# Optimization experiments

Hardware: AMD Instinct MI355X
Metric: run time of the kernel (lower is better)

## Reference

```python
import jax, jax.numpy as jnp
import numpy as np

D_MODEL = 512
NH_ATTN = 8
D_STATE = 64
HEADDIM = 128
D_INNER = 2 * D_MODEL          # 1024
NHEADS = D_INNER // HEADDIM    # 8
CONV_K = 4
CONV_DIM = D_INNER + 2 * D_STATE            # 1152
D_IN_PROJ = 2 * D_INNER + 2 * D_STATE + NHEADS  # 2184
B, S, M = 2, 2048, 1024
EPS = 1e-5


def setup_inputs() -> dict:
    key = jax.random.key(0)
    ks = jax.random.split(key, 10)
    s = 0.02
    return {
        'x': jax.random.normal(ks[0], (B, S, D_MODEL), dtype=jnp.float32),
        'memory': jax.random.normal(ks[1], (B, M, D_MODEL), dtype=jnp.float32),
        'pad_mask': jnp.ones((B, S, 1), dtype=jnp.float32),
        'ln1_g': jnp.ones((D_MODEL,)), 'ln1_b': jnp.zeros((D_MODEL,)),
        'ln2_g': jnp.ones((D_MODEL,)), 'ln2_b': jnp.zeros((D_MODEL,)),
        'W_in': jax.random.normal(ks[2], (D_IN_PROJ, D_MODEL)) * s,
        'conv_w': jax.random.normal(ks[3], (CONV_DIM, 1, CONV_K)) * s,
        'conv_b': jnp.zeros((CONV_DIM,)),
        'dt_bias': jnp.log(jnp.expm1(jax.random.uniform(ks[4], (NHEADS,), minval=0.001, maxval=0.1))),
        'A_log': jnp.log(jnp.arange(1, NHEADS + 1, dtype=jnp.float32)),
        'D_skip': jnp.ones((NHEADS,)),
        'rms_w': jnp.ones((D_INNER,)),
        'W_out': jax.random.normal(ks[5], (D_MODEL, D_INNER)) * s,
        'Wqkv': jax.random.normal(ks[6], (3 * D_MODEL, D_MODEL)) * s,
        'bqkv': jnp.zeros((3 * D_MODEL,)),
        'Wo': jax.random.normal(ks[7], (D_MODEL, D_MODEL)) * s,
        'bo': jnp.zeros((D_MODEL,)),
    }


def _layernorm(x, g, b):
    m = jnp.mean(x, axis=-1, keepdims=True)
    v = jnp.mean((x - m) ** 2, axis=-1, keepdims=True)
    return (x - m) * jax.lax.rsqrt(v + EPS) * g + b


def _mamba(x, W_in, conv_w, conv_b, dt_bias, A_log, D_skip, rms_w, W_out):
    b, s, _ = x.shape
    zxbcdt = x @ W_in.T                                     # [b,s,2184]
    z, xBC, dt = jnp.split(zxbcdt, [D_INNER, D_INNER + CONV_DIM], axis=-1)
    # causal depthwise conv over time on (x, B, C)
    xt = jnp.transpose(xBC, (0, 2, 1))                      # [b,C,s]
    xt = jax.lax.conv_general_dilated(
        xt, conv_w, (1,), [(CONV_K - 1, 0)],
        feature_group_count=CONV_DIM,
        dimension_numbers=('NCH', 'OIH', 'NCH'))
    xBC = jax.nn.silu(jnp.transpose(xt, (0, 2, 1)) + conv_b)
    xs, Bm, Cm = jnp.split(xBC, [D_INNER, D_INNER + D_STATE], axis=-1)
    dt = jax.nn.softplus(dt + dt_bias)                      # [b,s,H]
    A = -jnp.exp(A_log)                                     # [H]
    xh = xs.reshape(b, s, NHEADS, HEADDIM)                  # [b,s,H,P]

    def step(h, inps):
        dt_t, B_t, C_t, x_t = inps                          # [b,H],[b,N],[b,N],[b,H,P]
        decay = jnp.exp(dt_t * A)                           # [b,H]
        h = h * decay[..., None, None] + (dt_t[..., None, None] * x_t[..., None]) * B_t[:, None, None, :]
        y = jnp.einsum('bhpn,bn->bhp', h, C_t)
        return h, y

    h0 = jnp.zeros((b, NHEADS, HEADDIM, D_STATE), dtype=x.dtype)
    _, ys = jax.lax.scan(step, h0, (dt.transpose(1, 0, 2), Bm.transpose(1, 0, 2),
                                    Cm.transpose(1, 0, 2), xh.transpose(1, 0, 2, 3)))
    y = ys.transpose(1, 0, 2, 3) + D_skip[None, None, :, None] * xh
    y = y.reshape(b, s, D_INNER) * jax.nn.silu(z)           # gated
    y = y * jax.lax.rsqrt(jnp.mean(y * y, axis=-1, keepdims=True) + EPS) * rms_w
    return y @ W_out.T


def _cross_attn(q_in, memory, Wqkv, bqkv, Wo, bo):
    b, s, _ = q_in.shape
    m = memory.shape[1]
    dh = D_MODEL // NH_ATTN
    q = (q_in @ Wqkv[:D_MODEL].T + bqkv[:D_MODEL]).reshape(b, s, NH_ATTN, dh)
    k = (memory @ Wqkv[D_MODEL:2 * D_MODEL].T + bqkv[D_MODEL:2 * D_MODEL]).reshape(b, m, NH_ATTN, dh)
    v = (memory @ Wqkv[2 * D_MODEL:].T + bqkv[2 * D_MODEL:]).reshape(b, m, NH_ATTN, dh)
    scores = jnp.einsum('bqhd,bkhd->bhqk', q, k) / jnp.sqrt(jnp.asarray(dh, q.dtype))
    p = jax.nn.softmax(scores, axis=-1)
    out = jnp.einsum('bhqk,bkhd->bqhd', p, v).reshape(b, s, D_MODEL)
    return out @ Wo.T + bo


def reference(x, memory, pad_mask, ln1_g, ln1_b, ln2_g, ln2_b, W_in, conv_w, conv_b,
              dt_bias, A_log, D_skip, rms_w, W_out, Wqkv, bqkv, Wo, bo):
    residual = x
    xn = _layernorm(x, ln1_g, ln1_b) * pad_mask
    x = residual + _mamba(xn, W_in, conv_w, conv_b, dt_bias, A_log, D_skip, rms_w, W_out)
    h = _layernorm(x, ln2_g, ln2_b)
    x = x + _cross_attn(h, memory, Wqkv, bqkv, Wo, bo)
    return x
```

## Files before the change

kernel.cpp:

```cpp
#include <hip/hip_runtime.h>
#include <hip/hip_bf16.h>

typedef __hip_bfloat16 bf16;
typedef short v8s __attribute__((ext_vector_type(8)));
typedef short v4s __attribute__((ext_vector_type(4)));
typedef float v4f __attribute__((ext_vector_type(4)));

__device__ __forceinline__ void gll16(const bf16* g, bf16* l) {
    __builtin_amdgcn_global_load_lds(
        (const __attribute__((address_space(1))) unsigned int*)g,
        (__attribute__((address_space(3))) unsigned int*)l, 16, 0, 0);
}
__device__ __forceinline__ float bf2f(short s) {
    return __uint_as_float(((unsigned int)(unsigned short)s) << 16);
}
__device__ __forceinline__ short f2bfs(float f) {
    return (short)__bfloat16_as_ushort(__float2bfloat16(f));
}

__global__ __launch_bounds__(256) void pre_kernel(
    const float* __restrict__ x, const float* __restrict__ g,
    const float* __restrict__ bt, const float* __restrict__ mask,
    bf16* __restrict__ xn,
    const float* __restrict__ W_in, const float* __restrict__ W_out,
    const float* __restrict__ Wqkv, const float* __restrict__ Wo,
    const float* __restrict__ mem,
    bf16* __restrict__ Winb, bf16* __restrict__ Woutb, bf16* __restrict__ Wqkvb,
    bf16* __restrict__ Wob, bf16* __restrict__ memb)
{
    int tid = threadIdx.x;
    if (blockIdx.x < 4096) {
        int row = blockIdx.x;
        const float* xr = x + (size_t)row * 512;
        float v0 = xr[tid], v1 = xr[tid + 256];
        float s = v0 + v1, ss = v0 * v0 + v1 * v1;
        #pragma unroll
        for (int o = 32; o; o >>= 1) { s += __shfl_xor(s, o); ss += __shfl_xor(ss, o); }
        __shared__ float l1[4], l2[4];
        if ((tid & 63) == 0) { l1[tid >> 6] = s; l2[tid >> 6] = ss; }
        __syncthreads();
        s = l1[0] + l1[1] + l1[2] + l1[3];
        ss = l2[0] + l2[1] + l2[2] + l2[3];
        float mean = s * (1.f / 512.f);
        float var = ss * (1.f / 512.f) - mean * mean;
        float rs = rsqrtf(var + 1e-5f);
        float mk = mask[row];
        xn[(size_t)row * 512 + tid] =
            __float2bfloat16(((v0 - mean) * rs * g[tid] + bt[tid]) * mk);
        xn[(size_t)row * 512 + tid + 256] =
            __float2bfloat16(((v1 - mean) * rs * g[tid + 256] + bt[tid + 256]) * mk);
        return;
    }
    int i = (blockIdx.x - 4096) * 256 + tid;
    const int E0 = 2184 * 512;
    const int E1 = E0 + 524288;
    const int E2 = E1 + 786432;
    const int E3 = E2 + 262144;
    const int E4 = E3 + 1048576;
    if (i < E0) {
        Winb[i] = __float2bfloat16(W_in[i]);
    } else if (i < E1) {
        int j = i - E0; Woutb[j] = __float2bfloat16(W_out[j]);
    } else if (i < E2) {
        int j = i - E1; Wqkvb[j] = __float2bfloat16(Wqkv[j]);
    } else if (i < E3) {
        int j = i - E2; Wob[j] = __float2bfloat16(Wo[j]);
    } else if (i < E4) {
        int j = i - E3; memb[j] = __float2bfloat16(mem[j]);
    }
}

__global__ __launch_bounds__(256) void ln_kernel(
    const bf16* __restrict__ x, const float* __restrict__ g,
    const float* __restrict__ bt, bf16* __restrict__ out)
{
    int row = blockIdx.x, tid = threadIdx.x;
    const bf16* xr = x + (size_t)row * 512;
    unsigned int pk = *(const unsigned int*)(xr + tid * 2);
    float v0 = bf2f((short)(pk & 0xffff));
    float v1 = bf2f((short)(pk >> 16));
    float s = v0 + v1, ss = v0 * v0 + v1 * v1;
    #pragma unroll
    for (int o = 32; o; o >>= 1) { s += __shfl_xor(s, o); ss += __shfl_xor(ss, o); }
    __shared__ float l1[4], l2[4];
    if ((tid & 63) == 0) { l1[tid >> 6] = s; l2[tid >> 6] = ss; }
    __syncthreads();
    s = l1[0] + l1[1] + l1[2] + l1[3];
    ss = l2[0] + l2[1] + l2[2] + l2[3];
    float mean = s * (1.f / 512.f);
    float var = ss * (1.f / 512.f) - mean * mean;
    float rs = rsqrtf(var + 1e-5f);
    int i0 = tid * 2;
    unsigned int po =
        (unsigned int)(unsigned short)f2bfs((v0 - mean) * rs * g[i0] + bt[i0]) |
        ((unsigned int)(unsigned short)f2bfs((v1 - mean) * rs * g[i0 + 1] + bt[i0 + 1]) << 16);
    *(unsigned int*)(out + (size_t)row * 512 + i0) = po;
}

__global__ __launch_bounds__(256) void gemm_in(
    const bf16* __restrict__ A, const bf16* __restrict__ W, bf16* __restrict__ C)
{
    __shared__ bf16 lA[2][64 * 32];
    __shared__ bf16 lB[2][128 * 32];
    int bm = blockIdx.x * 64, bn = blockIdx.y * 128;
    int tid = threadIdx.x, lane = tid & 63, wv = tid >> 6;
    int wc = wv * 32;
    int lr15 = lane & 15, l4 = lane >> 4, lk8 = (lane >> 4) * 8;

    v4f acc[4][2] = {};
    int sr = tid >> 2, sc = (tid & 3) * 8;
    const bf16* Abase = A + (size_t)(bm + sr) * 512 + sc;
    const bf16* Wbase = W + (size_t)(bn + sr) * 512 + sc;

    int cur = 0;
    gll16(Abase, &lA[0][tid * 8]);
    gll16(Wbase, &lB[0][tid * 8]);
    gll16(Wbase + (size_t)64 * 512, &lB[0][tid * 8 + 2048]);
    __syncthreads();
    for (int t = 0; t < 16; ++t) {
        if (t + 1 < 16) {
            int k0 = (t + 1) * 32;
            gll16(Abase + k0, &lA[cur ^ 1][tid * 8]);
            gll16(Wbase + k0, &lB[cur ^ 1][tid * 8]);
            gll16(Wbase + (size_t)64 * 512 + k0, &lB[cur ^ 1][tid * 8 + 2048]);
        }
        v8s af[4], bfr[2];
        #pragma unroll
        for (int mi = 0; mi < 4; ++mi)
            af[mi] = *(const v8s*)&lA[cur][(mi * 16 + lr15) * 32 + lk8];
        #pragma unroll
        for (int ni = 0; ni < 2; ++ni)
            bfr[ni] = *(const v8s*)&lB[cur][(wc + ni * 16 + lr15) * 32 + lk8];
        #pragma unroll
        for (int mi = 0; mi < 4; ++mi)
            #pragma unroll
            for (int ni = 0; ni < 2; ++ni)
                acc[mi][ni] = __builtin_amdgcn_mfma_f32_16x16x32_bf16(
                    af[mi], bfr[ni], acc[mi][ni], 0, 0, 0);
        __syncthreads();
        cur ^= 1;
    }
    #pragma unroll
    for (int mi = 0; mi < 4; ++mi) {
        #pragma unroll
        for (int ni = 0; ni < 2; ++ni) {
            int col = bn + wc + ni * 16 + lr15;
            if (col < 2184) {
                #pragma unroll
                for (int r = 0; r < 4; ++r) {
                    int row = bm + mi * 16 + l4 * 4 + r;
                    C[(size_t)row * 2184 + col] = __float2bfloat16(acc[mi][ni][r]);
                }
            }
        }
    }
}

__global__ __launch_bounds__(256) void gemm64(
    const bf16* __restrict__ Aall, const bf16* __restrict__ Wall,
    const float* __restrict__ bias, const void* __restrict__ resid,
    void* __restrict__ Cout,
    int M, int N, int K, int ldA, int ldW, int ldC,
    long sA1, long sA2, long sW1, long sW2, long sC1, long sC2,
    int zdiv, int outbf16, int residbf16, bf16* __restrict__ vTout)
{
    __shared__ bf16 lA[2][64 * 32];
    __shared__ bf16 lB[2][64 * 32];
    int z = blockIdx.z;
    int zb = z / zdiv, zh = z - zb * zdiv;
    const bf16* A = Aall + zb * sA1 + zh * sA2;
    const bf16* W = Wall + zb * sW1 + zh * sW2;
    long coff = zb * sC1 + zh * sC2;

    int bm = blockIdx.x * 64, bn = blockIdx.y * 64;
    int tid = threadIdx.x, lane = tid & 63, wv = tid >> 6;
    int wr = (wv >> 1) * 32, wc = (wv & 1) * 32;
    int lr15 = lane & 15, lk8 = (lane >> 4) * 8;

    v4f acc[2][2] = {};
    int sr = tid >> 2, sc = (tid & 3) * 8;
    const bf16* Abase = A + (size_t)(bm + sr) * ldA + sc;
    const bf16* Wbase = W + (size_t)(bn + sr) * ldW + sc;

    int nt = K >> 5, cur = 0;
    gll16(Abase, &lA[0][tid * 8]);
    gll16(Wbase, &lB[0][tid * 8]);
    __syncthreads();
    for (int t = 0; t < nt; ++t) {
        if (t + 1 < nt) {
            int k0 = (t + 1) * 32;
            gll16(Abase + k0, &lA[cur ^ 1][tid * 8]);
            gll16(Wbase + k0, &lB[cur ^ 1][tid * 8]);
        }
        v8s a0 = *(const v8s*)&lA[cur][(wr + lr15) * 32 + lk8];
        v8s a1 = *(const v8s*)&lA[cur][(wr + 16 + lr15) * 32 + lk8];
        v8s b0 = *(const v8s*)&lB[cur][(wc + lr15) * 32 + lk8];
        v8s b1 = *(const v8s*)&lB[cur][(wc + 16 + lr15) * 32 + lk8];
        acc[0][0] = __builtin_amdgcn_mfma_f32_16x16x32_bf16(a0, b0, acc[0][0], 0, 0, 0);
        acc[0][1] = __builtin_amdgcn_mfma_f32_16x16x32_bf16(a0, b1, acc[0][1], 0, 0, 0);
        acc[1][0] = __builtin_amdgcn_mfma_f32_16x16x32_bf16(a1, b0, acc[1][0], 0, 0, 0);
        acc[1][1] = __builtin_amdgcn_mfma_f32_16x16x32_bf16(a1, b1, acc[1][1], 0, 0, 0);
        __syncthreads();
        cur ^= 1;
    }
    int r0 = bm + wr + (lane >> 4) * 4;
    int c0 = bn + wc + lr15;
    #pragma unroll
    for (int mi = 0; mi < 2; ++mi) {
        #pragma unroll
        for (int ni = 0; ni < 2; ++ni) {
            int col = c0 + ni * 16;
            if (col < N) {
                float bv = bias ? bias[col] : 0.f;
                float vals[4];
                #pragma unroll
                for (int r = 0; r < 4; ++r) {
                    int row = r0 + mi * 16 + r;
                    long idx = coff + (long)row * ldC + col;
                    float v = acc[mi][ni][r] + bv;
                    if (resid)
                        v += residbf16 ? bf2f(((const short*)resid)[idx])
                                       : ((const float*)resid)[idx];
                    vals[r] = v;
                    if (outbf16) ((bf16*)Cout)[idx] = __float2bfloat16(v);
                    else ((float*)Cout)[idx] = v;
                }
                if (vTout && col >= 512) {
                    int d = col - 512;
                    int row0 = r0 + mi * 16;
                    int bb = row0 >> 10, m0 = row0 & 1023;
                    v4s pk;
                    #pragma unroll
                    for (int r = 0; r < 4; ++r) pk[r] = f2bfs(vals[r]);
                    *(v4s*)(vTout + (((size_t)(bb * 8 + (d >> 6)) * 64 + (d & 63))
                                     * 1024 + m0)) = pk;
                }
            }
        }
    }
}

__global__ __launch_bounds__(256) void qkv_proj(
    const bf16* __restrict__ hb, const bf16* __restrict__ memb,
    const bf16* __restrict__ Wqkvb, const float* __restrict__ bqkv,
    bf16* __restrict__ qb, bf16* __restrict__ kvb, bf16* __restrict__ vTout)
{
    __shared__ bf16 lA[2][64 * 32];
    __shared__ bf16 lB[2][64 * 32];
    const bf16* A; const bf16* W; const float* bias; bf16* C;
    int bm, bn, ldA, ldC;
    bf16* vT = nullptr;
    if (blockIdx.z == 0) {
        A = hb; W = Wqkvb; bias = bqkv; C = qb;
        bm = blockIdx.x * 64; bn = blockIdx.y * 64;
        ldA = 512; ldC = 512;
    } else {
        int id = blockIdx.y * 64 + blockIdx.x;
        A = memb; W = Wqkvb + 512 * 512; bias = bqkv + 512; C = kvb;
        bm = (id & 31) * 64; bn = (id >> 5) * 64;
        ldA = 512; ldC = 1024;
        vT = vTout;
    }
    int tid = threadIdx.x, lane = tid & 63, wv = tid >> 6;
    int wr = (wv >> 1) * 32, wc = (wv & 1) * 32;
    int lr15 = lane & 15, lk8 = (lane >> 4) * 8;

    v4f acc[2][2] = {};
    int sr = tid >> 2, sc = (tid & 3) * 8;
    const bf16* Abase = A + (size_t)(bm + sr) * ldA + sc;
    const bf16* Wbase = W + (size_t)(bn + sr) * 512 + sc;

    int cur = 0;
    gll16(Abase, &lA[0][tid * 8]);
    gll16(Wbase, &lB[0][tid * 8]);
    __syncthreads();
    for (int t = 0; t < 16; ++t) {
        if (t + 1 < 16) {
            int k0 = (t + 1) * 32;
            gll16(Abase + k0, &lA[cur ^ 1][tid * 8]);
            gll16(Wbase + k0, &lB[cur ^ 1][tid * 8]);
        }
        v8s a0 = *(const v8s*)&lA[cur][(wr + lr15) * 32 + lk8];
        v8s a1 = *(const v8s*)&lA[cur][(wr + 16 + lr15) * 32 + lk8];
        v8s b0 = *(const v8s*)&lB[cur][(wc + lr15) * 32 + lk8];
        v8s b1 = *(const v8s*)&lB[cur][(wc + 16 + lr15) * 32 + lk8];
        acc[0][0] = __builtin_amdgcn_mfma_f32_16x16x32_bf16(a0, b0, acc[0][0], 0, 0, 0);
        acc[0][1] = __builtin_amdgcn_mfma_f32_16x16x32_bf16(a0, b1, acc[0][1], 0, 0, 0);
        acc[1][0] = __builtin_amdgcn_mfma_f32_16x16x32_bf16(a1, b0, acc[1][0], 0, 0, 0);
        acc[1][1] = __builtin_amdgcn_mfma_f32_16x16x32_bf16(a1, b1, acc[1][1], 0, 0, 0);
        __syncthreads();
        cur ^= 1;
    }
    int r0 = bm + wr + (lane >> 4) * 4;
    int c0 = bn + wc + lr15;
    #pragma unroll
    for (int mi = 0; mi < 2; ++mi) {
        #pragma unroll
        for (int ni = 0; ni < 2; ++ni) {
            int col = c0 + ni * 16;
            float bv = bias[col];
            float vals[4];
            #pragma unroll
            for (int r = 0; r < 4; ++r) {
                int row = r0 + mi * 16 + r;
                float v = acc[mi][ni][r] + bv;
                vals[r] = v;
                C[(size_t)row * ldC + col] = __float2bfloat16(v);
            }
            if (vT && col >= 512) {
                int d = col - 512;
                int row0 = r0 + mi * 16;
                int bb = row0 >> 10, m0 = row0 & 1023;
                v4s pk;
                #pragma unroll
                for (int r = 0; r < 4; ++r) pk[r] = f2bfs(vals[r]);
                *(v4s*)(vT + (((size_t)(bb * 8 + (d >> 6)) * 64 + (d & 63))
                              * 1024 + m0)) = pk;
            }
        }
    }
}

__global__ __launch_bounds__(256) void flash_attn(
    const bf16* __restrict__ qb, const bf16* __restrict__ kvb,
    const bf16* __restrict__ vT, bf16* __restrict__ attn)
{
    __shared__ bf16 lK[2][128 * 64];
    __shared__ bf16 lV[2][64 * 128];
    __shared__ bf16 lP[4][16 * 128];
    int z = blockIdx.z;
    int b = z >> 3, h = z & 7;
    int q0 = blockIdx.x * 64;
    int tid = threadIdx.x, lane = tid & 63, wv = tid >> 6;
    int l15 = lane & 15, l4 = lane >> 4, l7 = lane & 7;

    const bf16* Qg = qb + (size_t)(b * 2048 + q0) * 512 + h * 64;
    const bf16* Kg = kvb + (size_t)b * 1024 * 1024 + h * 64;
    const bf16* Vg = vT + (size_t)z * 64 * 1024;

    v8s af[2];
    #pragma unroll
    for (int ks = 0; ks < 2; ++ks)
        af[ks] = *(const v8s*)(Qg + (size_t)(wv * 16 + l15) * 512 + (ks * 4 + l4) * 8);

    #pragma unroll
    for (int pass = 0; pass < 4; ++pass) {
        int s = pass * 256 + tid;
        int kr = s >> 3, kc = s & 7;
        gll16(Kg + (size_t)kr * 1024 + ((kc ^ (kr & 7)) << 3), &lK[0][s * 8]);
        int vr = s >> 4, vc = s & 15;
        int vsw = (vc & 8) | ((vc & 7) ^ (vr & 7));
        gll16(Vg + (size_t)vr * 1024 + (vsw << 3), &lV[0][s * 8]);
    }
    __syncthreads();

    v4f o[4] = {};
    v4f l_run = (v4f){0.f, 0.f, 0.f, 0.f};
    bf16* lPw = &lP[wv][0];

    int cur = 0;
    #pragma unroll 1
    for (int t = 0; t < 8; ++t) {
        if (t + 1 < 8) {
            int k0n = (t + 1) * 128;
            #pragma unroll
            for (int pass = 0; pass < 4; ++pass) {
                int s = pass * 256 + tid;
                int kr = s >> 3, kc = s & 7;
                gll16(Kg + (size_t)(k0n + kr) * 1024 + ((kc ^ (kr & 7)) << 3),
                      &lK[cur ^ 1][s * 8]);
                int vr = s >> 4, vc = s & 15;
                int vsw = (vc & 8) | ((vc & 7) ^ (vr & 7));
                gll16(Vg + (size_t)vr * 1024 + k0n + (vsw << 3), &lV[cur ^ 1][s * 8]);
            }
        }
        v4f s_acc[8];
        #pragma unroll
        for (int kn = 0; kn < 8; ++kn) {
            s_acc[kn] = (v4f){0.f, 0.f, 0.f, 0.f};
            #pragma unroll
            for (int ks = 0; ks < 2; ++ks) {
                v8s kv = *(const v8s*)&lK[cur][(kn * 16 + l15) * 64 +
                                               (((ks * 4 + l4) ^ l7) << 3)];
                s_acc[kn] = __builtin_amdgcn_mfma_f32_16x16x32_bf16(
                    af[ks], kv, s_acc[kn], 0, 0, 0);
            }
        }
        v4f rs = {0.f, 0.f, 0.f, 0.f};
        #pragma unroll
        for (int kn = 0; kn < 8; ++kn)
            #pragma unroll
            for (int r = 0; r < 4; ++r) {
                float pv = __expf(0.125f * s_acc[kn][r]);
                s_acc[kn][r] = pv;
                rs[r] += pv;
            }
        #pragma unroll
        for (int off = 8; off >= 1; off >>= 1)
            #pragma unroll
            for (int r = 0; r < 4; ++r)
                rs[r] += __shfl_xor(rs[r], off);
        #pragma unroll
        for (int r = 0; r < 4; ++r)
            l_run[r] += rs[r];
        #pragma unroll
        for (int kn = 0; kn < 8; ++kn)
            #pragma unroll
            for (int r = 0; r < 4; ++r) {
                int row = l4 * 4 + r;
                int col = kn * 16 + l15;
                int c = col >> 3;
                int csw = (c & 8) | ((c & 7) ^ (row & 7));
                lPw[row * 128 + (csw << 3) + (col & 7)] =
                    __float2bfloat16(s_acc[kn][r]);
            }
        #pragma unroll
        for (int ni = 0; ni < 4; ++ni)
            #pragma unroll
            for (int ks = 0; ks < 4; ++ks) {
                int ck = ks * 4 + l4;
                int psw = (ck & 8) | ((ck & 7) ^ l7);
                v8s pv = *(const v8s*)&lPw[l15 * 128 + (psw << 3)];
                v8s vv = *(const v8s*)&lV[cur][(ni * 16 + l15) * 128 + (psw << 3)];
                o[ni] = __builtin_amdgcn_mfma_f32_16x16x32_bf16(
                    pv, vv, o[ni], 0, 0, 0);
            }
        __syncthreads();
        cur ^= 1;
    }
    v4f inv;
    #pragma unroll
    for (int r = 0; r < 4; ++r) inv[r] = 1.f / l_run[r];
    #pragma unroll
    for (int ni = 0; ni < 4; ++ni)
        #pragma unroll
        for (int r = 0; r < 4; ++r) {
            int row = q0 + wv * 16 + l4 * 4 + r;
            int col = h * 64 + ni * 16 + l15;
            attn[(size_t)(b * 2048 + row) * 512 + col] =
                __float2bfloat16(o[ni][r] * inv[r]);
        }
}

__global__ __launch_bounds__(256) void conv_dt(
    const bf16* __restrict__ zx, const float* __restrict__ cw,
    const float* __restrict__ cb, bf16* __restrict__ out,
    const float* __restrict__ dt_bias, const float* __restrict__ A_log,
    float* __restrict__ dtb, float* __restrict__ decb)
{
    int tid = threadIdx.x;
    if (blockIdx.x >= 576) {
        int i = (blockIdx.x - 576) * 256 + tid;
        if (i >= 32768) return;
        int h = i & 7, row = i >> 3;
        float d = bf2f(((const short*)zx)[(size_t)row * 2184 + 2176 + h]) + dt_bias[h];
        float sp = d > 20.f ? d : log1pf(expf(d));
        dtb[i] = sp;
        decb[i] = expf(-expf(A_log[h]) * sp);
        return;
    }
    int idx = blockIdx.x * 256 + tid;
    int c4 = (idx % 288) * 4;
    int tb = (idx / 288) % 256;
    int b  = idx / (288 * 256);
    int t0 = tb * 8;
    const bf16* base = zx + (size_t)b * 2048 * 2184 + 1024 + c4;
    bf16* ob = out + ((size_t)(b * 2048 + t0)) * 1152 + c4;

    float wt[4][4];
    #pragma unroll
    for (int k = 0; k < 4; ++k)
        #pragma unroll
        for (int j = 0; j < 4; ++j) wt[j][k] = cw[(c4 + k) * 4 + j];
    v4f bias = *(const v4f*)(cb + c4);

    v4f r[11];
    #pragma unroll
    for (int j = 0; j < 11; ++j) {
        int ts = t0 - 3 + j;
        if (ts >= 0) {
            v4s raw = *(const v4s*)(base + (size_t)ts * 2184);
            #pragma unroll
            for (int k = 0; k < 4; ++k) r[j][k] = bf2f(raw[k]);
        } else r[j] = (v4f){0.f, 0.f, 0.f, 0.f};
    }
    #pragma unroll
    for (int t = 0; t < 8; ++t) {
        v4f acc = bias;
        #pragma unroll
        for (int k = 0; k < 4; ++k)
            acc[k] += wt[0][k] * r[t][k] + wt[1][k] * r[t + 1][k]
                    + wt[2][k] * r[t + 2][k] + wt[3][k] * r[t + 3][k];
        v4s res;
        #pragma unroll
        for (int k = 0; k < 4; ++k) {
            float v = acc[k] / (1.f + expf(-acc[k]));
            res[k] = f2bfs(v);
        }
        *(v4s*)(ob + (size_t)t * 1152) = res;
    }
}

__global__ __launch_bounds__(256) void scan_p1(
    const bf16* __restrict__ conv, const float* __restrict__ dtb,
    const float* __restrict__ decb, const float* __restrict__ A_log,
    bf16* __restrict__ slocal, float* __restrict__ cdec)
{
    int chunk = blockIdx.x, bh = blockIdx.y;
    int b = bh >> 3, h = bh & 7;
    int tid = threadIdx.x;
    int wv = tid >> 6, lane = tid & 63;
    int nh = lane >> 5, psub = lane & 31;
    int p = wv * 32 + psub;
    __shared__ float lx[64][128];
    __shared__ float lB[64][64];
    __shared__ float ldt[64], ldec[64];
    const bf16* cb_ = conv + (size_t)b * 2048 * 1152;
    int t0 = chunk * 64;
    #pragma unroll
    for (int pass = 0; pass < 4; ++pass) {
        int s = pass * 256 + tid;
        int row = s >> 4, c8 = (s & 15) * 8;
        v8s raw = *(const v8s*)(cb_ + (size_t)(t0 + row) * 1152 + h * 128 + c8);
        v4f lo, hi;
        #pragma unroll
        for (int j = 0; j < 4; ++j) { lo[j] = bf2f(raw[j]); hi[j] = bf2f(raw[j + 4]); }
        *(v4f*)&lx[row][c8] = lo;
        *(v4f*)&lx[row][c8 + 4] = hi;
    }
    #pragma unroll
    for (int pass = 0; pass < 2; ++pass) {
        int s = pass * 256 + tid;
        int row = s >> 3, c8 = (s & 7) * 8;
        v8s raw = *(const v8s*)(cb_ + (size_t)(t0 + row) * 1152 + 1024 + c8);
        v4f lo, hi;
        #pragma unroll
        for (int j = 0; j < 4; ++j) { lo[j] = bf2f(raw[j]); hi[j] = bf2f(raw[j + 4]); }
        *(v4f*)&lB[row][c8] = lo;
        *(v4f*)&lB[row][c8 + 4] = hi;
    }
    if (tid < 64) {
        int ri = (b * 2048 + t0 + tid) * 8 + h;
        ldt[tid] = dtb[ri]; ldec[tid] = decb[ri];
    }
    __syncthreads();
    v4f hs[8] = {};
    float sdt = 0.f;
    #pragma unroll 2
    for (int t = 0; t < 64; ++t) {
        float dtv = ldt[t], dec = ldec[t];
        float c1 = dtv * lx[t][p];
        const v4f* Bp = (const v4f*)&lB[t][nh * 32];
        #pragma unroll
        for (int i = 0; i < 8; ++i) hs[i] = hs[i] * dec + Bp[i] * c1;
        sdt += dtv;
    }
    if (tid == 0) cdec[bh * 32 + chunk] = expf(-expf(A_log[h]) * sdt);
    bf16* S = slocal + ((size_t)bh * 32 + chunk) * 8192;
    #pragma unroll
    for (int i = 0; i < 8; ++i)
        #pragma unroll
        for (int j = 0; j < 4; ++j)
            S[(nh * 32 + i * 4 + j) * 128 + p] = __float2bfloat16(hs[i][j]);
}

__global__ __launch_bounds__(256) void scan_comb(
    const bf16* __restrict__ slocal, const float* __restrict__ cdec,
    bf16* __restrict__ hinit)
{
    int e = blockIdx.x * 256 + threadIdx.x;
    int bh = e >> 12, np2 = e & 4095;
    size_t base = (size_t)bh * 262144 + (size_t)np2 * 2;
    const float* cd = cdec + bh * 32;
    float h0 = 0.f, h1 = 0.f;
    for (int c = 0; c < 32; ++c) {
        size_t idx = base + (size_t)c * 8192;
        unsigned int raw = *(const unsigned int*)(slocal + idx);
        unsigned int pk = (unsigned int)(unsigned short)f2bfs(h0) |
                          ((unsigned int)(unsigned short)f2bfs(h1) << 16);
        *(unsigned int*)(hinit + idx) = pk;
        float cdv = cd[c];
        h0 = h0 * cdv + bf2f((short)(raw & 0xffff));
        h1 = h1 * cdv + bf2f((short)(raw >> 16));
    }
}

__global__ __launch_bounds__(256) void scan_p3(
    const bf16* __restrict__ conv, const float* __restrict__ dtb,
    const float* __restrict__ decb, const bf16* __restrict__ hinit,
    const float* __restrict__ Dskip, bf16* __restrict__ ybuf)
{
    int chunk = blockIdx.x, bh = blockIdx.y;
    int b = bh >> 3, h = bh & 7;
    int tid = threadIdx.x;
    int wv = tid >> 6, lane = tid & 63;
    int nh = lane >> 5, psub = lane & 31;
    int p = wv * 32 + psub;
    __shared__ float lx[64][128];
    __shared__ float lB[64][64];
    __shared__ float lC[64][64];
    __shared__ float ldt[64], ldec[64];
    const bf16* cb_ = conv + (size_t)b * 2048 * 1152;
    int t0 = chunk * 64;
    #pragma unroll
    for (int pass = 0; pass < 4; ++pass) {
        int s = pass * 256 + tid;
        int row = s >> 4, c8 = (s & 15) * 8;
        v8s raw = *(const v8s*)(cb_ + (size_t)(t0 + row) * 1152 + h * 128 + c8);
        v4f lo, hi;
        #pragma unroll
        for (int j = 0; j < 4; ++j) { lo[j] = bf2f(raw[j]); hi[j] = bf2f(raw[j + 4]); }
        *(v4f*)&lx[row][c8] = lo;
        *(v4f*)&lx[row][c8 + 4] = hi;
    }
    #pragma unroll
    for (int pass = 0; pass < 2; ++pass) {
        int s = pass * 256 + tid;
        int row = s >> 3, c8 = (s & 7) * 8;
        v8s rawB = *(const v8s*)(cb_ + (size_t)(t0 + row) * 1152 + 1024 + c8);
        v8s rawC = *(const v8s*)(cb_ + (size_t)(t0 + row) * 1152 + 1088 + c8);
        v4f lo, hi;
        #pragma unroll
        for (int j = 0; j < 4; ++j) { lo[j] = bf2f(rawB[j]); hi[j] = bf2f(rawB[j + 4]); }
        *(v4f*)&lB[row][c8] = lo;
        *(v4f*)&lB[row][c8 + 4] = hi;
        #pragma unroll
        for (int j = 0; j < 4; ++j) { lo[j] = bf2f(rawC[j]); hi[j] = bf2f(rawC[j + 4]); }
        *(v4f*)&lC[row][c8] = lo;
        *(v4f*)&lC[row][c8 + 4] = hi;
    }
    if (tid < 64) {
        int ri = (b * 2048 + t0 + tid) * 8 + h;
        ldt[tid] = dtb[ri]; ldec[tid] = decb[ri];
    }
    __syncthreads();
    v4f hs[8];
    const bf16* H = hinit + ((size_t)bh * 32 + chunk) * 8192;
    #pragma unroll
    for (int i = 0; i < 8; ++i)
        #pragma unroll
        for (int j = 0; j < 4; ++j)
            hs[i][j] = __bfloat162float(H[(nh * 32 + i * 4 + j) * 128 + p]);
    float Dk = Dskip[h];
    #pragma unroll 2
    for (int t = 0; t < 64; ++t) {
        float dtv = ldt[t], dec = ldec[t];
        float xv = lx[t][p];
        float c1 = dtv * xv;
        const v4f* Bp = (const v4f*)&lB[t][nh * 32];
        const v4f* Cp = (const v4f*)&lC[t][nh * 32];
        v4f ya = {0.f, 0.f, 0.f, 0.f};
        #pragma unroll
        for (int i = 0; i < 8; ++i) {
            hs[i] = hs[i] * dec + Bp[i] * c1;
            ya += hs[i] * Cp[i];
        }
        float part = ya[0] + ya[1] + ya[2] + ya[3];
        part += __shfl_xor(part, 32);
        if (nh == 0)
            ybuf[((size_t)(b * 2048 + t0 + t)) * 1024 + h * 128 + p] =
                __float2bfloat16(part + Dk * xv);
    }
}

__global__ __launch_bounds__(256) void gate_rms(
    const bf16* __restrict__ ybuf, const bf16* __restrict__ zx,
    const float* __restrict__ rms_w, bf16* __restrict__ out)
{
    int row = blockIdx.x, tid = threadIdx.x;
    int i0 = tid * 4;
    v4s yv = *(const v4s*)(ybuf + (size_t)row * 1024 + i0);
    v4s zv = *(const v4s*)(zx + (size_t)row * 2184 + i0);
    v4f rw = *(const v4f*)(rms_w + i0);
    float vals[4];
    float ss = 0.f;
    #pragma unroll
    for (int j = 0; j < 4; ++j) {
        float y = bf2f(yv[j]);
        float z = bf2f(zv[j]);
        float g = y * (z / (1.f + expf(-z)));
        vals[j] = g;
        ss += g * g;
    }
    #pragma unroll
    for (int o = 32; o; o >>= 1) ss += __shfl_xor(ss, o);
    __shared__ float l[4];
    if ((tid & 63) == 0) l[tid >> 6] = ss;
    __syncthreads();
    ss = l[0] + l[1] + l[2] + l[3];
    float rs = rsqrtf(ss * (1.f / 1024.f) + 1e-5f);
    v4s o4;
    #pragma unroll
    for (int j = 0; j < 4; ++j)
        o4[j] = f2bfs(vals[j] * rs * rw[j]);
    *(v4s*)(out + (size_t)row * 1024 + i0) = o4;
}

extern "C" void kernel_launch(void* const* d_in, const int* in_sizes, int n_in,
                              void* d_out, int out_size, void* d_ws, size_t ws_size,
                              hipStream_t stream) {
    (void)in_sizes; (void)n_in; (void)out_size; (void)ws_size;
    const float* x       = (const float*)d_in[0];
    const float* memory  = (const float*)d_in[1];
    const float* mask    = (const float*)d_in[2];
    const float* ln1_g   = (const float*)d_in[3];
    const float* ln1_b   = (const float*)d_in[4];
    const float* ln2_g   = (const float*)d_in[5];
    const float* ln2_b   = (const float*)d_in[6];
    const float* W_in    = (const float*)d_in[7];
    const float* conv_w  = (const float*)d_in[8];
    const float* conv_b  = (const float*)d_in[9];
    const float* dt_bias = (const float*)d_in[10];
    const float* A_log   = (const float*)d_in[11];
    const float* D_skip  = (const float*)d_in[12];
    const float* rms_w   = (const float*)d_in[13];
    const float* W_out   = (const float*)d_in[14];
    const float* Wqkv    = (const float*)d_in[15];
    const float* bqkv    = (const float*)d_in[16];
    const float* Wo      = (const float*)d_in[17];
    const float* bo      = (const float*)d_in[18];
    float* out = (float*)d_out;

    char* w = (char*)d_ws;
    bf16*  xn     = (bf16*)(w + 0);
    bf16*  Winb   = (bf16*)(w + 4194304);
    bf16*  Woutb  = (bf16*)(w + 6430720);
    bf16*  Wqkvb  = (bf16*)(w + 7479296);
    bf16*  Wob    = (bf16*)(w + 9052160);
    bf16*  memb   = (bf16*)(w + 9576448);
    bf16*  zx     = (bf16*)(w + 11673600);
    bf16*  gout   = (bf16*)(w + 29564928);
    bf16*  conv   = (bf16*)(w + 47456256);
    float* dtb    = (float*)(w + 66330624);
    float* decb   = (float*)(w + 66461696);
    bf16*  ybuf   = (bf16*)(w + 66592768);
    bf16*  slocal = (bf16*)(w + 83369984);
    bf16*  hinit  = (bf16*)(w + 91758592);
    bf16*  x2b    = (bf16*)(w + 100147200);
    bf16*  hb     = (bf16*)(w + 108535808);
    bf16*  qb     = (bf16*)(w + 112730112);
    float* cdec   = (float*)(w + 116924416);
    bf16*  kvb    = (bf16*)(w + 116928512);
    bf16*  vT     = (bf16*)(w + 121122816);
    bf16*  attn   = (bf16*)(w + 123219968);

    pre_kernel<<<18704, 256, 0, stream>>>(x, ln1_g, ln1_b, mask, xn,
                                          W_in, W_out, Wqkv, Wo, memory,
                                          Winb, Woutb, Wqkvb, Wob, memb);

    gemm_in<<<dim3(64, 18), 256, 0, stream>>>(xn, Winb, zx);

    conv_dt<<<704, 256, 0, stream>>>(zx, conv_w, conv_b, conv,
                                     dt_bias, A_log, dtb, decb);

    scan_p1<<<dim3(32, 16), 256, 0, stream>>>(conv, dtb, decb, A_log, slocal, cdec);
    scan_comb<<<256, 256, 0, stream>>>(slocal, cdec, hinit);
    scan_p3<<<dim3(32, 16), 256, 0, stream>>>(conv, dtb, decb, hinit, D_skip, ybuf);

    gate_rms<<<4096, 256, 0, stream>>>(ybuf, zx, rms_w, gout);

    gemm64<<<dim3(64, 8, 1), 256, 0, stream>>>(
        gout, Woutb, nullptr, (const void*)x, (void*)x2b,
        4096, 512, 1024, 1024, 1024, 512,
        0, 0, 0, 0, 0, 0, 1, 1, 0, nullptr);

    ln_kernel<<<4096, 256, 0, stream>>>(x2b, ln2_g, ln2_b, hb);

    qkv_proj<<<dim3(64, 8, 2), 256, 0, stream>>>(hb, memb, Wqkvb, bqkv,
                                                 qb, kvb, vT);

    flash_attn<<<dim3(32, 1, 16), 256, 0, stream>>>(qb, kvb, vT, attn);

    gemm64<<<dim3(64, 8, 1), 256, 0, stream>>>(
        attn, Wob, bo, (const void*)x2b, (void*)out,
        4096, 512, 512, 512, 512, 512,
        0, 0, 0, 0, 0, 0, 1, 0, 1, nullptr);
}
```

Baseline: 175.2 us.

## Fuse causal conv, SiLU and dt softplus into scan kernels

Removes the separate conv_dt kernel and recomputes the depthwise causal conv plus SiLU, along with the dt softplus and decay, directly inside scan_p1 and scan_p3 from the zx projection output. This drops one launch and the write and re-read of the intermediate conv, dtb and decb buffers. In exchange, both scan kernels redo the conv, reading four shifted taps per row, so B and x-channel work is duplicated. The change also switches to the fast __expf.

```diff
diff --git a/kernel.cpp b/kernel.cpp
--- a/kernel.cpp
+++ b/kernel.cpp
@@ -442,68 +442,10 @@
         }
 }
 
-__global__ __launch_bounds__(256) void conv_dt(
+__global__ __launch_bounds__(256) void scan_p1(
     const bf16* __restrict__ zx, const float* __restrict__ cw,
-    const float* __restrict__ cb, bf16* __restrict__ out,
-    const float* __restrict__ dt_bias, const float* __restrict__ A_log,
-    float* __restrict__ dtb, float* __restrict__ decb)
-{
-    int tid = threadIdx.x;
-    if (blockIdx.x >= 576) {
-        int i = (blockIdx.x - 576) * 256 + tid;
-        if (i >= 32768) return;
-        int h = i & 7, row = i >> 3;
-        float d = bf2f(((const short*)zx)[(size_t)row * 2184 + 2176 + h]) + dt_bias[h];
-        float sp = d > 20.f ? d : log1pf(expf(d));
-        dtb[i] = sp;
-        decb[i] = expf(-expf(A_log[h]) * sp);
-        return;
-    }
-    int idx = blockIdx.x * 256 + tid;
-    int c4 = (idx % 288) * 4;
-    int tb = (idx / 288) % 256;
-    int b  = idx / (288 * 256);
-    int t0 = tb * 8;
-    const bf16* base = zx + (size_t)b * 2048 * 2184 + 1024 + c4;
-    bf16* ob = out + ((size_t)(b * 2048 + t0)) * 1152 + c4;
-
-    float wt[4][4];
-    #pragma unroll
-    for (int k = 0; k < 4; ++k)
-        #pragma unroll
-        for (int j = 0; j < 4; ++j) wt[j][k] = cw[(c4 + k) * 4 + j];
-    v4f bias = *(const v4f*)(cb + c4);
-
-    v4f r[11];
-    #pragma unroll
-    for (int j = 0; j < 11; ++j) {
-        int ts = t0 - 3 + j;
-        if (ts >= 0) {
-            v4s raw = *(const v4s*)(base + (size_t)ts * 2184);
-            #pragma unroll
-            for (int k = 0; k < 4; ++k) r[j][k] = bf2f(raw[k]);
-        } else r[j] = (v4f){0.f, 0.f, 0.f, 0.f};
-    }
-    #pragma unroll
-    for (int t = 0; t < 8; ++t) {
-        v4f acc = bias;
-        #pragma unroll
-        for (int k = 0; k < 4; ++k)
-            acc[k] += wt[0][k] * r[t][k] + wt[1][k] * r[t + 1][k]
-                    + wt[2][k] * r[t + 2][k] + wt[3][k] * r[t + 3][k];
-        v4s res;
-        #pragma unroll
-        for (int k = 0; k < 4; ++k) {
-            float v = acc[k] / (1.f + expf(-acc[k]));
-            res[k] = f2bfs(v);
-        }
-        *(v4s*)(ob + (size_t)t * 1152) = res;
-    }
-}
-
-__global__ __launch_bounds__(256) void scan_p1(
-    const bf16* __restrict__ conv, const float* __restrict__ dtb,
-    const float* __restrict__ decb, const float* __restrict__ A_log,
+    const float* __restrict__ cb, const float* __restrict__ dt_bias,
+    const float* __restrict__ A_log,
     bf16* __restrict__ slocal, float* __restrict__ cdec)
 {
     int chunk = blockIdx.x, bh = blockIdx.y;
@@ -515,33 +457,82 @@
     __shared__ float lx[64][128];
     __shared__ float lB[64][64];
     __shared__ float ldt[64], ldec[64];
-    const bf16* cb_ = conv + (size_t)b * 2048 * 1152;
+    const bf16* zb_ = zx + (size_t)b * 2048 * 2184;
     int t0 = chunk * 64;
-    #pragma unroll
-    for (int pass = 0; pass < 4; ++pass) {
-        int s = pass * 256 + tid;
-        int row = s >> 4, c8 = (s & 15) * 8;
-        v8s raw = *(const v8s*)(cb_ + (size_t)(t0 + row) * 1152 + h * 128 + c8);
-        v4f lo, hi;
-        #pragma unroll
-        for (int j = 0; j < 4; ++j) { lo[j] = bf2f(raw[j]); hi[j] = bf2f(raw[j + 4]); }
-        *(v4f*)&lx[row][c8] = lo;
-        *(v4f*)&lx[row][c8 + 4] = hi;
-    }
-    #pragma unroll
-    for (int pass = 0; pass < 2; ++pass) {
-        int s = pass * 256 + tid;
-        int row = s >> 3, c8 = (s & 7) * 8;
-        v8s raw = *(const v8s*)(cb_ + (size_t)(t0 + row) * 1152 + 1024 + c8);
-        v4f lo, hi;
-        #pragma unroll
-        for (int j = 0; j < 4; ++j) { lo[j] = bf2f(raw[j]); hi[j] = bf2f(raw[j + 4]); }
-        *(v4f*)&lB[row][c8] = lo;
-        *(v4f*)&lB[row][c8 + 4] = hi;
+
+    {
+        int c8x = (tid & 15) * 8;
+        v4f wx[8]; float cbx[8];
+        #pragma unroll
+        for (int k = 0; k < 8; ++k) {
+            wx[k] = *(const v4f*)(cw + (h * 128 + c8x + k) * 4);
+            cbx[k] = cb[h * 128 + c8x + k];
+        }
+        #pragma unroll
+        for (int pass = 0; pass < 4; ++pass) {
+            int row = pass * 16 + (tid >> 4);
+            v8s tap[4];
+            #pragma unroll
+            for (int j = 0; j < 4; ++j) {
+                int zr = t0 + row - 3 + j;
+                tap[j] = (zr >= 0) ? *(const v8s*)(zb_ + (size_t)zr * 2184 + 1024 +
+                                                   h * 128 + c8x)
+                                   : (v8s){0, 0, 0, 0, 0, 0, 0, 0};
+            }
+            #pragma unroll
+            for (int half = 0; half < 2; ++half) {
+                v4f r;
+                #pragma unroll
+                for (int k4 = 0; k4 < 4; ++k4) {
+                    int k = half * 4 + k4;
+                    float a = cbx[k];
+                    #pragma unroll
+                    for (int j = 0; j < 4; ++j) a += wx[k][j] * bf2f(tap[j][k]);
+                    r[k4] = a / (1.f + __expf(-a));
+                }
+                *(v4f*)&lx[row][c8x + half * 4] = r;
+            }
+        }
+    }
+    {
+        int c8b = (tid & 7) * 8;
+        v4f wB[8]; float cbB[8];
+        #pragma unroll
+        for (int k = 0; k < 8; ++k) {
+            wB[k] = *(const v4f*)(cw + (1024 + c8b + k) * 4);
+            cbB[k] = cb[1024 + c8b + k];
+        }
+        #pragma unroll
+        for (int pass = 0; pass < 2; ++pass) {
+            int row = pass * 32 + (tid >> 3);
+            v8s tap[4];
+            #pragma unroll
+            for (int j = 0; j < 4; ++j) {
+                int zr = t0 + row - 3 + j;
+                tap[j] = (zr >= 0) ? *(const v8s*)(zb_ + (size_t)zr * 2184 + 2048 + c8b)
+                                   : (v8s){0, 0, 0, 0, 0, 0, 0, 0};
+            }
+            #pragma unroll
+            for (int half = 0; half < 2; ++half) {
+                v4f r;
+                #pragma unroll
+                for (int k4 = 0; k4 < 4; ++k4) {
+                    int k = half * 4 + k4;
+                    float a = cbB[k];
+                    #pragma unroll
+                    for (int j = 0; j < 4; ++j) a += wB[k][j] * bf2f(tap[j][k]);
+                    r[k4] = a / (1.f + __expf(-a));
+                }
+                *(v4f*)&lB[row][c8b + half * 4] = r;
+            }
+        }
     }
     if (tid < 64) {
-        int ri = (b * 2048 + t0 + tid) * 8 + h;
-        ldt[tid] = dtb[ri]; ldec[tid] = decb[ri];
+        float d = bf2f(((const short*)zb_)[(size_t)(t0 + tid) * 2184 + 2176 + h])
+                  + dt_bias[tid * 0 + h];
+        float sp = d > 20.f ? d : log1pf(__expf(d));
+        ldt[tid] = sp;
+        ldec[tid] = __expf(-__expf(A_log[h]) * sp);
     }
     __syncthreads();
     v4f hs[8] = {};
@@ -586,8 +577,9 @@
 }
 
 __global__ __launch_bounds__(256) void scan_p3(
-    const bf16* __restrict__ conv, const float* __restrict__ dtb,
-    const float* __restrict__ decb, const bf16* __restrict__ hinit,
+    const bf16* __restrict__ zx, const float* __restrict__ cw,
+    const float* __restrict__ cb, const float* __restrict__ dt_bias,
+    const float* __restrict__ A_log, const bf16* __restrict__ hinit,
     const float* __restrict__ Dskip, bf16* __restrict__ ybuf)
 {
     int chunk = blockIdx.x, bh = blockIdx.y;
@@ -600,38 +592,94 @@
     __shared__ float lB[64][64];
     __shared__ float lC[64][64];
     __shared__ float ldt[64], ldec[64];
-    const bf16* cb_ = conv + (size_t)b * 2048 * 1152;
+    const bf16* zb_ = zx + (size_t)b * 2048 * 2184;
     int t0 = chunk * 64;
-    #pragma unroll
-    for (int pass = 0; pass < 4; ++pass) {
-        int s = pass * 256 + tid;
-        int row = s >> 4, c8 = (s & 15) * 8;
-        v8s raw = *(const v8s*)(cb_ + (size_t)(t0 + row) * 1152 + h * 128 + c8);
-        v4f lo, hi;
-        #pragma unroll
-        for (int j = 0; j < 4; ++j) { lo[j] = bf2f(raw[j]); hi[j] = bf2f(raw[j + 4]); }
-        *(v4f*)&lx[row][c8] = lo;
-        *(v4f*)&lx[row][c8 + 4] = hi;
-    }
-    #pragma unroll
-    for (int pass = 0; pass < 2; ++pass) {
-        int s = pass * 256 + tid;
-        int row = s >> 3, c8 = (s & 7) * 8;
-        v8s rawB = *(const v8s*)(cb_ + (size_t)(t0 + row) * 1152 + 1024 + c8);
-        v8s rawC = *(const v8s*)(cb_ + (size_t)(t0 + row) * 1152 + 1088 + c8);
-        v4f lo, hi;
-        #pragma unroll
-        for (int j = 0; j < 4; ++j) { lo[j] = bf2f(rawB[j]); hi[j] = bf2f(rawB[j + 4]); }
-        *(v4f*)&lB[row][c8] = lo;
-        *(v4f*)&lB[row][c8 + 4] = hi;
-        #pragma unroll
-        for (int j = 0; j < 4; ++j) { lo[j] = bf2f(rawC[j]); hi[j] = bf2f(rawC[j + 4]); }
-        *(v4f*)&lC[row][c8] = lo;
-        *(v4f*)&lC[row][c8 + 4] = hi;
+
+    {
+        int c8x = (tid & 15) * 8;
+        v4f wx[8]; float cbx[8];
+        #pragma unroll
+        for (int k = 0; k < 8; ++k) {
+            wx[k] = *(const v4f*)(cw + (h * 128 + c8x + k) * 4);
+            cbx[k] = cb[h * 128 + c8x + k];
+        }
+        #pragma unroll
+        for (int pass = 0; pass < 4; ++pass) {
+            int row = pass * 16 + (tid >> 4);
+            v8s tap[4];
+            #pragma unroll
+            for (int j = 0; j < 4; ++j) {
+                int zr = t0 + row - 3 + j;
+                tap[j] = (zr >= 0) ? *(const v8s*)(zb_ + (size_t)zr * 2184 + 1024 +
+                                                   h * 128 + c8x)
+                                   : (v8s){0, 0, 0, 0, 0, 0, 0, 0};
+            }
+            #pragma unroll
+            for (int half = 0; half < 2; ++half) {
+                v4f r;
+                #pragma unroll
+                for (int k4 = 0; k4 < 4; ++k4) {
+                    int k = half * 4 + k4;
+                    float a = cbx[k];
+                    #pragma unroll
+                    for (int j = 0; j < 4; ++j) a += wx[k][j] * bf2f(tap[j][k]);
+                    r[k4] = a / (1.f + __expf(-a));
+                }
+                *(v4f*)&lx[row][c8x + half * 4] = r;
+            }
+        }
+    }
+    {
+        int c8b = (tid & 7) * 8;
+        v4f wB[8], wC[8]; float cbB[8], cbC[8];
+        #pragma unroll
+        for (int k = 0; k < 8; ++k) {
+            wB[k] = *(const v4f*)(cw + (1024 + c8b + k) * 4);
+            cbB[k] = cb[1024 + c8b + k];
+            wC[k] = *(const v4f*)(cw + (1088 + c8b + k) * 4);
+            cbC[k] = cb[1088 + c8b + k];
+        }
+        #pragma unroll
+        for (int pass = 0; pass < 2; ++pass) {
+            int row = pass * 32 + (tid >> 3);
+            v8s tapB[4], tapC[4];
+            #pragma unroll
+            for (int j = 0; j < 4; ++j) {
+                int zr = t0 + row - 3 + j;
+                if (zr >= 0) {
+                    tapB[j] = *(const v8s*)(zb_ + (size_t)zr * 2184 + 2048 + c8b);
+                    tapC[j] = *(const v8s*)(zb_ + (size_t)zr * 2184 + 2112 + c8b);
+                } else {
+                    tapB[j] = (v8s){0, 0, 0, 0, 0, 0, 0, 0};
+                    tapC[j] = (v8s){0, 0, 0, 0, 0, 0, 0, 0};
+                }
+            }
+            #pragma unroll
+            for (int half = 0; half < 2; ++half) {
+                v4f rB, rC;
+                #pragma unroll
+                for (int k4 = 0; k4 < 4; ++k4) {
+                    int k = half * 4 + k4;
+                    float a = cbB[k];
+                    #pragma unroll
+                    for (int j = 0; j < 4; ++j) a += wB[k][j] * bf2f(tapB[j][k]);
+                    rB[k4] = a / (1.f + __expf(-a));
+                    float c = cbC[k];
+                    #pragma unroll
+                    for (int j = 0; j < 4; ++j) c += wC[k][j] * bf2f(tapC[j][k]);
+                    rC[k4] = c / (1.f + __expf(-c));
+                }
+                *(v4f*)&lB[row][c8b + half * 4] = rB;
+                *(v4f*)&lC[row][c8b + half * 4] = rC;
+            }
+        }
     }
     if (tid < 64) {
-        int ri = (b * 2048 + t0 + tid) * 8 + h;
-        ldt[tid] = dtb[ri]; ldec[tid] = decb[ri];
+        float d = bf2f(((const short*)zb_)[(size_t)(t0 + tid) * 2184 + 2176 + h])
+                  + dt_bias[h];
+        float sp = d > 20.f ? d : log1pf(__expf(d));
+        ldt[tid] = sp;
+        ldec[tid] = __expf(-__expf(A_log[h]) * sp);
     }
     __syncthreads();
     v4f hs[8];
@@ -730,9 +778,6 @@
     bf16*  memb   = (bf16*)(w + 9576448);
     bf16*  zx     = (bf16*)(w + 11673600);
     bf16*  gout   = (bf16*)(w + 29564928);
-    bf16*  conv   = (bf16*)(w + 47456256);
-    float* dtb    = (float*)(w + 66330624);
-    float* decb   = (float*)(w + 66461696);
     bf16*  ybuf   = (bf16*)(w + 66592768);
     bf16*  slocal = (bf16*)(w + 83369984);
     bf16*  hinit  = (bf16*)(w + 91758592);
@@ -750,12 +795,11 @@
 
     gemm_in<<<dim3(64, 18), 256, 0, stream>>>(xn, Winb, zx);
 
-    conv_dt<<<704, 256, 0, stream>>>(zx, conv_w, conv_b, conv,
-                                     dt_bias, A_log, dtb, decb);
-
-    scan_p1<<<dim3(32, 16), 256, 0, stream>>>(conv, dtb, decb, A_log, slocal, cdec);
+    scan_p1<<<dim3(32, 16), 256, 0, stream>>>(zx, conv_w, conv_b, dt_bias, A_log,
+                                              slocal, cdec);
     scan_comb<<<256, 256, 0, stream>>>(slocal, cdec, hinit);
-    scan_p3<<<dim3(32, 16), 256, 0, stream>>>(conv, dtb, decb, hinit, D_skip, ybuf);
+    scan_p3<<<dim3(32, 16), 256, 0, stream>>>(zx, conv_w, conv_b, dt_bias, A_log,
+                                              hinit, D_skip, ybuf);
 
     gate_rms<<<4096, 256, 0, stream>>>(ybuf, zx, rms_w, gout);
 
```

Result: slower. 182.6 us (+4.2%).
